# Kernel optimization log

Measured on AMD Instinct MI355X. Metric: run time of the kernel, lower is better.

The kernel has to match this reference:

```python
import jax, jax.numpy as jnp
import numpy as np

SEQ_LEN = 1024
D_MODEL = 512
K_FILT = 24
HEADS = 8
R = 512  # must equal d_model for the module's forward to type-check
NFFT = 2048  # nearest power of two >= 2*SEQ_LEN-1
LN_EPS = 1e-5


def _spectral_filters():
    # Hankel matrix Z[i,j] = 2 / ((i+j)^3 - (i+j)), i,j in 1..T
    e = np.arange(1, SEQ_LEN + 1, dtype=np.float64)
    ipj = e[:, None] + e[None, :]
    Z = 2.0 / (ipj ** 3 - ipj)
    sigma, phi = np.linalg.eigh(Z)
    sigma_k = np.clip(sigma[-K_FILT:], 1e-9, None)
    phi_k = phi[:, -K_FILT:] * sigma_k ** 0.25
    return phi_k.astype(np.float32)  # (T, K)


def setup_inputs() -> dict:
    key = jax.random.key(0)
    ks = jax.random.split(key, 12)
    s = 0.02
    B = 2

    def lin(k):
        kw, kb = jax.random.split(k)
        return (jax.random.normal(kw, (D_MODEL, D_MODEL), jnp.float32) * s,
                jax.random.normal(kb, (D_MODEL,), jnp.float32) * s)

    Wq, bq = lin(ks[0]); Wk, bk = lin(ks[1]); Wv, bv = lin(ks[2])
    Wg, bg = lin(ks[3]); Wo, bo = lin(ks[4])
    return {
        'x': jax.random.normal(ks[5], (B, SEQ_LEN, D_MODEL), jnp.float32),
        'stu_filters': jnp.asarray(_spectral_filters()),
        'M_inputs': jax.random.normal(ks[6], (D_MODEL, R), jnp.float32) * s,
        'M_filters': jax.random.normal(ks[7], (K_FILT, R), jnp.float32) * s,
        'Wq': Wq, 'bq': bq, 'Wk': Wk, 'bk': bk, 'Wv': Wv, 'bv': bv,
        'Wg': Wg, 'bg': bg, 'Wo': Wo, 'bo': bo,
        'ln_w': jnp.ones((R,), jnp.float32),
        'ln_b': jnp.zeros((R,), jnp.float32),
    }


def _stu_conv(u, v):
    # u: (B, T, r), v: (T, r). FFT-based causal conv with sign featurization.
    T = u.shape[1]
    sgn = jnp.where(jnp.arange(T) % 2 == 1, -1.0, 1.0)[None, :, None]  # (1,T,1)
    Vf = jnp.fft.rfft(v[None, :, :, None], n=NFFT, axis=1)  # (1,F,r,1)
    U = jnp.stack([u, u * sgn], axis=-1)  # (B,T,r,2)
    Uf = jnp.fft.rfft(U, n=NFFT, axis=1)  # (B,F,r,2)
    conv = jnp.fft.irfft(Vf * Uf, n=NFFT, axis=1)[:, :T]  # (B,T,r,2)
    return conv[..., 0], conv[..., 1] * sgn


def _layernorm(x, w, b):
    mu = jnp.mean(x, axis=-1, keepdims=True)
    var = jnp.mean((x - mu) ** 2, axis=-1, keepdims=True)
    return (x - mu) * jax.lax.rsqrt(var + LN_EPS) * w + b


def reference(x, stu_filters, M_inputs, M_filters, Wq, bq, Wk, bk, Wv, bv,
              Wg, bg, Wo, bo, ln_w, ln_b):
    B, T, d = x.shape
    hd = d // HEADS
    # STU features
    u_proj = x @ M_inputs                    # (B,T,r)
    phi_proj = stu_filters @ M_filters       # (T,r)
    sp, sm = _stu_conv(u_proj, phi_proj)
    x_tilde = _layernorm(sp + sm, ln_w, ln_b)  # (B,T,r==d)
    # gated linear attention with gelu features and causal cumsum state
    def proj(W, b):
        y = (x @ W.T + b).reshape(B, T, HEADS, hd).transpose(0, 2, 1, 3)
        return jax.nn.gelu(y, approximate=True)
    Q = proj(Wq, bq); K = proj(Wk, bk); V = proj(Wv, bv)
    Zt = jnp.einsum('bhtp,bhtn->bhtpn', V, K)   # (B,H,T,hd,hd)
    Hc = jnp.cumsum(Zt, axis=2)
    Y = jnp.einsum('bhtp,bhtpn->bhtn', Q, Hc)   # (B,H,T,hd)
    Y_attn = Y.transpose(0, 2, 1, 3).reshape(B, T, d)
    gate = jax.nn.sigmoid(x @ Wg.T + bg)
    comb = gate * Y_attn + (1.0 - gate) * x_tilde
    return comb @ Wo.T + bo
```

## Files before the change

### kernel.cpp

```cpp
#include <hip/hip_runtime.h>
#include <hip/hip_bf16.h>

#define T_SEQ 1024
#define D_MOD 512
#define NHEAD 8
#define HDIM  64
#define R_DIM 512
#define BATCH 2

typedef __attribute__((ext_vector_type(8))) __bf16 bf16x8;
typedef __attribute__((ext_vector_type(4))) float f32x4;

__device__ __forceinline__ float ldin(const void* p, size_t i, int bf) {
    if (bf) return __bfloat162float(((const __hip_bfloat16*)p)[i]);
    return ((const float*)p)[i];
}
__device__ __forceinline__ void stout(void* p, size_t i, int bf, float v) {
    if (bf) ((__hip_bfloat16*)p)[i] = __float2bfloat16(v);
    else    ((float*)p)[i] = v;
}

__device__ __forceinline__ float gelu_f(float x) {
    return 0.5f * x * (1.f + tanhf(0.7978845608028654f * (x + 0.044715f * x * x * x)));
}

__device__ __forceinline__ int detect_bf(const void* x) {
    __shared__ int cnt;
    if (threadIdx.x == 0) cnt = 0;
    __syncthreads();
    const unsigned short* h = (const unsigned short*)x;
    int c = 0;
    for (int i = threadIdx.x; i < 8192; i += 256)
        if ((h[i] & 0x7F80u) == 0x7F80u) c++;
    if (c) atomicAdd(&cnt, c);
    __syncthreads();
    return cnt == 0;
}

__global__ __launch_bounds__(256) void mega_gemm(
    const void* __restrict__ x, const void* __restrict__ Mi,
    const void* __restrict__ stf, const void* __restrict__ Mf,
    const void* __restrict__ Wq, const void* __restrict__ bq,
    const void* __restrict__ Wk, const void* __restrict__ bk,
    const void* __restrict__ Wv, const void* __restrict__ bv,
    const void* __restrict__ Wg, const void* __restrict__ bg,
    float* __restrict__ fu, float* __restrict__ fphi,
    __bf16* __restrict__ fQ, __bf16* __restrict__ fKT,
    __bf16* __restrict__ fV, __bf16* __restrict__ fG)
{
    const int tid = threadIdx.x;
    const int job = blockIdx.z;
    if (job == 6) {
        float4* zp = (float4*)(fphi + 524288);
        const int bid = blockIdx.y * 8 + blockIdx.x;
        const float4 z4 = make_float4(0.f, 0.f, 0.f, 0.f);
        #pragma unroll
        for (int q = 0; q < 8; ++q)
            zp[(size_t)bid * 2048 + q * 256 + tid] = z4;
        return;
    }
    const int bf = detect_bf(x);
    const void* A = x; const void* Bw; const void* bias = nullptr;
    int Kd = 512, act = 0; bool trb = true;
    switch (job) {
        case 0: Bw = Mi; trb = false; break;
        case 1: Bw = Wq; bias = bq; act = 1; break;
        case 2: Bw = Wk; bias = bk; act = 1; break;
        case 3: Bw = Wv; bias = bv; act = 1; break;
        case 4: Bw = Wg; bias = bg; act = 2; break;
        default: A = stf; Bw = Mf; trb = false; Kd = 32; break;
    }
    const int M = (job == 5) ? 1024 : 2048;
    const int m0 = blockIdx.y * 64;
    if (m0 >= M) return;
    const int n0 = blockIdx.x * 64;

    __shared__ __align__(16) __bf16 sm[2 * 64 * 40];
    __bf16 (*As)[40] = (__bf16 (*)[40])sm;
    __bf16 (*Bs)[40] = (__bf16 (*)[40])(sm + 64 * 40);
    const int wave = tid >> 6, lane = tid & 63;
    const int lm = lane & 15, kq = lane >> 4;

    f32x4 acc[4] = {};

    for (int k0 = 0; k0 < Kd; k0 += 32) {
        if (k0) __syncthreads();
        {
            const int mo = tid >> 2;
            const int ko = (tid & 3) * 8;
            if (job == 5) {
                bf16x8 t;
                #pragma unroll
                for (int q = 0; q < 8; ++q) {
                    const int k = ko + q;
                    t[q] = (k < 24) ? (__bf16)ldin(A, (size_t)(m0 + mo) * 24 + k, bf)
                                    : (__bf16)0.f;
                }
                *(bf16x8*)&As[mo][ko] = t;
            } else if (bf) {
                *(bf16x8*)&As[mo][ko] =
                    *(const bf16x8*)((const __bf16*)A + (size_t)(m0 + mo) * 512 + k0 + ko);
            } else {
                const float* Af = (const float*)A + (size_t)(m0 + mo) * 512 + k0 + ko;
                const float4 f0 = *(const float4*)Af;
                const float4 f1 = *(const float4*)(Af + 4);
                bf16x8 t;
                t[0]=(__bf16)f0.x; t[1]=(__bf16)f0.y; t[2]=(__bf16)f0.z; t[3]=(__bf16)f0.w;
                t[4]=(__bf16)f1.x; t[5]=(__bf16)f1.y; t[6]=(__bf16)f1.z; t[7]=(__bf16)f1.w;
                *(bf16x8*)&As[mo][ko] = t;
            }
        }
        if (trb) {
            const int no = tid >> 2;
            const int ko = (tid & 3) * 8;
            const size_t go = (size_t)(n0 + no) * 512 + k0 + ko;
            if (bf) {
                *(bf16x8*)&Bs[no][ko] = *(const bf16x8*)((const __bf16*)Bw + go);
            } else {
                const float* Bf = (const float*)Bw + go;
                const float4 f0 = *(const float4*)Bf;
                const float4 f1 = *(const float4*)(Bf + 4);
                bf16x8 t;
                t[0]=(__bf16)f0.x; t[1]=(__bf16)f0.y; t[2]=(__bf16)f0.z; t[3]=(__bf16)f0.w;
                t[4]=(__bf16)f1.x; t[5]=(__bf16)f1.y; t[6]=(__bf16)f1.z; t[7]=(__bf16)f1.w;
                *(bf16x8*)&Bs[no][ko] = t;
            }
        } else {
            const int n = tid & 63;
            const int kk = (tid >> 6) * 8;
            bf16x8 t;
            #pragma unroll
            for (int e = 0; e < 8; ++e) {
                const int k = k0 + kk + e;
                t[e] = (job == 5 && k >= 24) ? (__bf16)0.f
                     : (__bf16)ldin(Bw, (size_t)k * 512 + n0 + n, bf);
            }
            *(bf16x8*)&Bs[n][kk] = t;
        }
        __syncthreads();
        const bf16x8 a = *(const bf16x8*)&As[wave * 16 + lm][kq * 8];
        #pragma unroll
        for (int nt = 0; nt < 4; ++nt) {
            const bf16x8 b = *(const bf16x8*)&Bs[nt * 16 + lm][kq * 8];
            acc[nt] = __builtin_amdgcn_mfma_f32_16x16x32_bf16(a, b, acc[nt], 0, 0, 0);
        }
    }
    if (job == 2) {
        __syncthreads();
        __bf16 (*Kt)[72] = (__bf16 (*)[72])sm;
        #pragma unroll
        for (int nt = 0; nt < 4; ++nt) {
            const int n = nt * 16 + lm;
            #pragma unroll
            for (int r2 = 0; r2 < 4; ++r2) {
                float v = acc[nt][r2] + ldin(bias, (size_t)(n0 + n), bf);
                Kt[n][wave * 16 + kq * 4 + r2] = (__bf16)gelu_f(v);
            }
        }
        __syncthreads();
        const int h = n0 >> 6;
        const int b = m0 >> 10;
        const int tb = m0 & 1023;
        #pragma unroll
        for (int q = 0; q < 2; ++q) {
            const int c = q * 256 + tid;
            const int p = c >> 3, off = (c & 7) * 8;
            *(bf16x8*)&fKT[(((size_t)b * NHEAD + h) * 64 + p) * T_SEQ + tb + off] =
                *(const bf16x8*)&Kt[p][off];
        }
        return;
    }
    #pragma unroll
    for (int nt = 0; nt < 4; ++nt) {
        const int n = n0 + nt * 16 + lm;
        #pragma unroll
        for (int r2 = 0; r2 < 4; ++r2) {
            const int m = m0 + wave * 16 + kq * 4 + r2;
            float v = acc[nt][r2];
            if (bias) v += ldin(bias, (size_t)n, bf);
            if (act == 1) v = gelu_f(v);
            if (act == 2) v = 1.f / (1.f + expf(-v));
            switch (job) {
                case 0: fu[(size_t)m * 512 + n] = v; break;
                case 5: fphi[(size_t)m * 512 + n] = v; break;
                case 1: fQ[(size_t)m * 512 + n] = (__bf16)v; break;
                case 3: fV[(size_t)m * 512 + n] = (__bf16)v; break;
                default: fG[(size_t)m * 512 + n] = (__bf16)v; break;
            }
        }
    }
}

__global__ __launch_bounds__(256) void conv_attn_k(
    const float* __restrict__ u, const float* __restrict__ vphi,
    float* __restrict__ w,
    const __bf16* __restrict__ Q, const __bf16* __restrict__ KT,
    const __bf16* __restrict__ V, float* __restrict__ Y)
{
    __shared__ __align__(16) unsigned char smem[49152];
    const int tid = threadIdx.x;
    const int z = blockIdx.z;
    int rem = blockIdx.x, ti = 0;
    while (rem >= ((ti + 4) >> 2)) { rem -= (ti + 4) >> 2; ++ti; }
    const int jlo = rem * 4;
    const int jhi = (jlo + 3 < ti) ? jlo + 3 : ti;
    const int t0 = ti * 64;

    if (z < 2) {
        float (*vs)[64] = (float (*)[64])smem;
        float (*us)[64] = (float (*)[64])(smem + 16384);
        const int rl = tid & 63, tg = tid >> 6;
        const int b = z;
        const int r0 = blockIdx.y * 64;
        const float* ub = u + (size_t)b * T_SEQ * R_DIM;
        float acc[16] = {};
        for (int j = jlo; j <= jhi; ++j) {
            if (j != jlo) __syncthreads();
            const int L0 = j * 64;
            const int W0 = t0 - L0 - 63;
            #pragma unroll
            for (int jj = 0; jj < 8; ++jj) {
                const int n = jj * 256 + tid;
                const int row = n >> 4, c4 = (n & 15) * 4;
                int s = W0 + row;
                s = s < 0 ? 0 : (s > T_SEQ - 1 ? T_SEQ - 1 : s);
                *(float4*)&us[row][c4] = *(const float4*)&ub[(size_t)s * R_DIM + r0 + c4];
            }
            #pragma unroll
            for (int jj = 0; jj < 4; ++jj) {
                const int n = jj * 256 + tid;
                const int row = n >> 4, c4 = (n & 15) * 4;
                *(float4*)&vs[row][c4] = *(const float4*)&vphi[(size_t)(L0 + row) * R_DIM + r0 + c4];
            }
            __syncthreads();
            if (j < ti) {
                #pragma unroll
                for (int g = 0; g < 4; ++g) {
                    const int wsmin = tg * 16 + 49 - 16 * g;
                    float ur[30];
                    #pragma unroll
                    for (int q = 0; q < 30; ++q) ur[q] = us[wsmin + q][rl];
                    float vr[8];
                    #pragma unroll
                    for (int e = 0; e < 8; ++e) vr[e] = vs[16 * g + 2 * e][rl];
                    #pragma unroll
                    for (int e = 0; e < 8; ++e)
                        #pragma unroll
                        for (int i = 0; i < 16; ++i)
                            acc[i] += vr[e] * ur[i - 2 * e + 14];
                }
            } else {
                for (int l = 0; l < 64; l += 2) {
                    const float vv = vs[l][rl];
                    #pragma unroll
                    for (int i = 0; i < 16; ++i) {
                        const int srel = tg * 16 + i - l;
                        if (srel >= 0) acc[i] += vv * us[srel + 63][rl];
                    }
                }
            }
        }
        #pragma unroll
        for (int i = 0; i < 16; ++i)
            atomicAdd(&w[((size_t)b * T_SEQ + t0 + tg * 16 + i) * R_DIM + r0 + rl],
                      2.f * acc[i]);
    } else {
        __bf16 (*Qs)[72] = (__bf16 (*)[72])smem;
        __bf16 (*Vs)[72] = (__bf16 (*)[72])(smem + 9216);
        __bf16 (*Kt)[72] = (__bf16 (*)[72])(smem + 18432);
        __bf16 (*Sa)[72] = (__bf16 (*)[72])(smem + 27648);
        const int wave = tid >> 6, lane = tid & 63;
        const int lm = lane & 15, kq = lane >> 4;
        const int b = z - 2;
        const int h = blockIdx.y;
        const size_t cbase = ((size_t)b * T_SEQ) * D_MOD + h * HDIM;
        const __bf16* KTh = KT + (((size_t)b * NHEAD + h) * 64) * T_SEQ;
        #pragma unroll
        for (int it = 0; it < 2; ++it) {
            const int n = it * 256 + tid;
            const int row = n >> 3, p0 = (n & 7) * 8;
            *(bf16x8*)&Qs[row][p0] = *(const bf16x8*)&Q[cbase + (size_t)(t0 + row) * D_MOD + p0];
        }
        f32x4 accY[4] = {};
        for (int j = jlo; j <= jhi; ++j) {
            const int s0 = j * 64;
            __syncthreads();
            #pragma unroll
            for (int it = 0; it < 2; ++it) {
                const int n = it * 256 + tid;
                const int row = n >> 3, c0 = (n & 7) * 8;
                *(bf16x8*)&Vs[row][c0] = *(const bf16x8*)&V[cbase + (size_t)(s0 + row) * D_MOD + c0];
                *(bf16x8*)&Kt[row][c0] = *(const bf16x8*)&KTh[(size_t)row * T_SEQ + s0 + c0];
            }
            __syncthreads();
            f32x4 sacc[4] = {};
            #pragma unroll
            for (int ks = 0; ks < 2; ++ks) {
                const bf16x8 a = *(const bf16x8*)&Qs[wave * 16 + lm][ks * 32 + kq * 8];
                #pragma unroll
                for (int nt = 0; nt < 4; ++nt) {
                    const bf16x8 bb = *(const bf16x8*)&Vs[nt * 16 + lm][ks * 32 + kq * 8];
                    sacc[nt] = __builtin_amdgcn_mfma_f32_16x16x32_bf16(a, bb, sacc[nt], 0, 0, 0);
                }
            }
            const bool diag = (j == ti);
            #pragma unroll
            for (int nt = 0; nt < 4; ++nt) {
                const int sl = nt * 16 + lm;
                #pragma unroll
                for (int r2 = 0; r2 < 4; ++r2) {
                    const int tl = wave * 16 + kq * 4 + r2;
                    float v = sacc[nt][r2];
                    if (diag && sl > tl) v = 0.f;
                    Sa[tl][sl] = (__bf16)v;
                }
            }
            #pragma unroll
            for (int ks = 0; ks < 2; ++ks) {
                const bf16x8 a = *(const bf16x8*)&Sa[wave * 16 + lm][ks * 32 + kq * 8];
                #pragma unroll
                for (int nt = 0; nt < 4; ++nt) {
                    const bf16x8 bb = *(const bf16x8*)&Kt[nt * 16 + lm][ks * 32 + kq * 8];
                    accY[nt] = __builtin_amdgcn_mfma_f32_16x16x32_bf16(a, bb, accY[nt], 0, 0, 0);
                }
            }
        }
        #pragma unroll
        for (int nt = 0; nt < 4; ++nt) {
            const int nh = nt * 16 + lm;
            #pragma unroll
            for (int r2 = 0; r2 < 4; ++r2) {
                const int tl = wave * 16 + kq * 4 + r2;
                atomicAdd(&Y[cbase + (size_t)(t0 + tl) * D_MOD + nh], accY[nt][r2]);
            }
        }
    }
}

__global__ __launch_bounds__(256) void ln_k(float* __restrict__ w,
                                            const void* __restrict__ g,
                                            const void* __restrict__ b,
                                            const void* __restrict__ xref)
{
    const int bf = detect_bf(xref);
    const size_t row = (size_t)blockIdx.y * T_SEQ + blockIdx.x;
    float* p = w + row * R_DIM;
    const int tid = threadIdx.x;
    const float x0 = p[tid], x1 = p[tid + 256];
    __shared__ float red[4];
    float s = x0 + x1;
    #pragma unroll
    for (int off = 32; off > 0; off >>= 1) s += __shfl_down(s, off, 64);
    if ((tid & 63) == 0) red[tid >> 6] = s;
    __syncthreads();
    const float mu = (red[0] + red[1] + red[2] + red[3]) * (1.f / 512.f);
    __syncthreads();
    const float d0 = x0 - mu, d1 = x1 - mu;
    float vsum = d0 * d0 + d1 * d1;
    #pragma unroll
    for (int off = 32; off > 0; off >>= 1) vsum += __shfl_down(vsum, off, 64);
    if ((tid & 63) == 0) red[tid >> 6] = vsum;
    __syncthreads();
    const float var = (red[0] + red[1] + red[2] + red[3]) * (1.f / 512.f);
    const float rs = rsqrtf(var + 1e-5f);
    p[tid]       = d0 * rs * ldin(g, tid, bf)       + ldin(b, tid, bf);
    p[tid + 256] = d1 * rs * ldin(g, tid + 256, bf) + ldin(b, tid + 256, bf);
}

__global__ __launch_bounds__(256) void final_gemm(const __bf16* __restrict__ G,
                                                  const float* __restrict__ Yf,
                                                  const float* __restrict__ Xt,
                                                  const void* __restrict__ Wo,
                                                  const void* __restrict__ bo,
                                                  void* __restrict__ out,
                                                  const void* __restrict__ xref)
{
    const int bf = detect_bf(xref);
    __shared__ __align__(16) __bf16 As[64][40];
    __shared__ __align__(16) __bf16 Bs[64][40];
    const int tid = threadIdx.x;
    const int wave = tid >> 6, lane = tid & 63;
    const int lm = lane & 15, kq = lane >> 4;
    const int m0 = blockIdx.y * 64, n0 = blockIdx.x * 64;

    f32x4 acc[4] = {};

    for (int k0 = 0; k0 < 512; k0 += 32) {
        __syncthreads();
        {
            const int mo = tid >> 2;
            const int ko = (tid & 3) * 8;
            const size_t off = (size_t)(m0 + mo) * 512 + k0 + ko;
            const bf16x8 g8 = *(const bf16x8*)(G + off);
            const float4 y0 = *(const float4*)(Yf + off);
            const float4 y1 = *(const float4*)(Yf + off + 4);
            const float4 x0 = *(const float4*)(Xt + off);
            const float4 x1 = *(const float4*)(Xt + off + 4);
            const float yv[8] = {y0.x,y0.y,y0.z,y0.w,y1.x,y1.y,y1.z,y1.w};
            const float xv[8] = {x0.x,x0.y,x0.z,x0.w,x1.x,x1.y,x1.z,x1.w};
            bf16x8 t;
            #pragma unroll
            for (int q = 0; q < 8; ++q) {
                const float gg = (float)g8[q];
                t[q] = (__bf16)(gg * yv[q] + (1.f - gg) * xv[q]);
            }
            *(bf16x8*)&As[mo][ko] = t;
        }
        {
            const int no = tid >> 2;
            const int ko = (tid & 3) * 8;
            const size_t off = (size_t)(n0 + no) * 512 + k0 + ko;
            if (bf) {
                *(bf16x8*)&Bs[no][ko] = *(const bf16x8*)((const __bf16*)Wo + off);
            } else {
                const float* Bf = (const float*)Wo + off;
                const float4 f0 = *(const float4*)Bf;
                const float4 f1 = *(const float4*)(Bf + 4);
                bf16x8 t;
                t[0]=(__bf16)f0.x; t[1]=(__bf16)f0.y; t[2]=(__bf16)f0.z; t[3]=(__bf16)f0.w;
                t[4]=(__bf16)f1.x; t[5]=(__bf16)f1.y; t[6]=(__bf16)f1.z; t[7]=(__bf16)f1.w;
                *(bf16x8*)&Bs[no][ko] = t;
            }
        }
        __syncthreads();
        const bf16x8 a = *(const bf16x8*)&As[wave * 16 + lm][kq * 8];
        #pragma unroll
        for (int nt = 0; nt < 4; ++nt) {
            const bf16x8 b = *(const bf16x8*)&Bs[nt * 16 + lm][kq * 8];
            acc[nt] = __builtin_amdgcn_mfma_f32_16x16x32_bf16(a, b, acc[nt], 0, 0, 0);
        }
    }
    #pragma unroll
    for (int nt = 0; nt < 4; ++nt) {
        const int n = n0 + nt * 16 + lm;
        #pragma unroll
        for (int r2 = 0; r2 < 4; ++r2) {
            const int m = m0 + wave * 16 + kq * 4 + r2;
            float v = acc[nt][r2] + ldin(bo, (size_t)n, bf);
            stout(out, (size_t)m * 512 + n, bf, v);
        }
    }
}

extern "C" void kernel_launch(void* const* d_in, const int* in_sizes, int n_in,
                              void* d_out, int out_size, void* d_ws, size_t ws_size,
                              hipStream_t stream)
{
    const void* x   = d_in[0];
    const void* stf = d_in[1];
    const void* Mi  = d_in[2];
    const void* Mf  = d_in[3];
    const void* Wq  = d_in[4];  const void* bq = d_in[5];
    const void* Wk  = d_in[6];  const void* bk = d_in[7];
    const void* Wv  = d_in[8];  const void* bv = d_in[9];
    const void* Wg  = d_in[10]; const void* bg = d_in[11];
    const void* Wo  = d_in[12]; const void* bo = d_in[13];
    const void* lnw = d_in[14]; const void* lnb = d_in[15];

    float* base = (float*)d_ws;
    float*  f_u   = base;
    float*  f_phi = base + 1048576;
    float*  f_w   = base + 1572864;
    float*  f_Y   = base + 2621440;
    __bf16* f_Q   = (__bf16*)(base + 3670016);
    __bf16* f_KT  = f_Q + 1048576;
    __bf16* f_V   = f_KT + 1048576;
    __bf16* f_G   = f_V + 1048576;

    dim3 blk(256);

    mega_gemm<<<dim3(8, 32, 7), blk, 0, stream>>>(
        x, Mi, stf, Mf, Wq, bq, Wk, bk, Wv, bv, Wg, bg,
        f_u, f_phi, f_Q, f_KT, f_V, f_G);

    conv_attn_k<<<dim3(40, 8, 4), blk, 0, stream>>>(f_u, f_phi, f_w, f_Q, f_KT, f_V, f_Y);

    ln_k<<<dim3(T_SEQ, BATCH), blk, 0, stream>>>(f_w, lnw, lnb, x);

    final_gemm<<<dim3(8, 32), blk, 0, stream>>>(f_G, f_Y, f_w, Wo, bo, d_out, x);
}
```

Before: 204.2 us.

## Double-buffer LDS tiles and prefetch next K-slice in GEMM kernels

Both the multi-job projection GEMM and the final gated GEMM now use two shared-memory tile buffers. Global loads for the next K-slice are issued into registers before the MFMAs on the current slice, then written to the other buffer afterwards, with one barrier per iteration instead of two. This hides global-load latency behind compute, at the cost of twice the LDS and more live registers.

```diff
diff --git a/kernel.cpp b/kernel.cpp
--- a/kernel.cpp
+++ b/kernel.cpp
@@ -22,6 +22,13 @@
 
 __device__ __forceinline__ float gelu_f(float x) {
     return 0.5f * x * (1.f + tanhf(0.7978845608028654f * (x + 0.044715f * x * x * x)));
+}
+
+__device__ __forceinline__ bf16x8 cvt8(float4 a, float4 b) {
+    bf16x8 t;
+    t[0]=(__bf16)a.x; t[1]=(__bf16)a.y; t[2]=(__bf16)a.z; t[3]=(__bf16)a.w;
+    t[4]=(__bf16)b.x; t[5]=(__bf16)b.y; t[6]=(__bf16)b.z; t[7]=(__bf16)b.w;
+    return t;
 }
 
 __device__ __forceinline__ int detect_bf(const void* x) {
@@ -75,79 +82,86 @@
     if (m0 >= M) return;
     const int n0 = blockIdx.x * 64;
 
-    __shared__ __align__(16) __bf16 sm[2 * 64 * 40];
-    __bf16 (*As)[40] = (__bf16 (*)[40])sm;
-    __bf16 (*Bs)[40] = (__bf16 (*)[40])(sm + 64 * 40);
+    __shared__ __align__(16) __bf16 sm[2][2 * 64 * 40];
     const int wave = tid >> 6, lane = tid & 63;
     const int lm = lane & 15, kq = lane >> 4;
-
-    f32x4 acc[4] = {};
-
-    for (int k0 = 0; k0 < Kd; k0 += 32) {
-        if (k0) __syncthreads();
-        {
-            const int mo = tid >> 2;
-            const int ko = (tid & 3) * 8;
-            if (job == 5) {
-                bf16x8 t;
-                #pragma unroll
-                for (int q = 0; q < 8; ++q) {
-                    const int k = ko + q;
-                    t[q] = (k < 24) ? (__bf16)ldin(A, (size_t)(m0 + mo) * 24 + k, bf)
-                                    : (__bf16)0.f;
-                }
-                *(bf16x8*)&As[mo][ko] = t;
-            } else if (bf) {
-                *(bf16x8*)&As[mo][ko] =
-                    *(const bf16x8*)((const __bf16*)A + (size_t)(m0 + mo) * 512 + k0 + ko);
-            } else {
-                const float* Af = (const float*)A + (size_t)(m0 + mo) * 512 + k0 + ko;
-                const float4 f0 = *(const float4*)Af;
-                const float4 f1 = *(const float4*)(Af + 4);
-                bf16x8 t;
-                t[0]=(__bf16)f0.x; t[1]=(__bf16)f0.y; t[2]=(__bf16)f0.z; t[3]=(__bf16)f0.w;
-                t[4]=(__bf16)f1.x; t[5]=(__bf16)f1.y; t[6]=(__bf16)f1.z; t[7]=(__bf16)f1.w;
-                *(bf16x8*)&As[mo][ko] = t;
-            }
+    const int mo = tid >> 2, ko = (tid & 3) * 8;
+    const int gn = tid & 63, gk = (tid >> 6) * 8;
+
+    bf16x8 ba, bb;
+    float4 fa0, fa1, fb0, fb1;
+
+    auto issue = [&](int k0) {
+        if (job == 5) {
+            bf16x8 t;
+            #pragma unroll
+            for (int q = 0; q < 8; ++q) {
+                const int k = ko + q;
+                t[q] = (k < 24) ? (__bf16)ldin(A, (size_t)(m0 + mo) * 24 + k, bf)
+                                : (__bf16)0.f;
+            }
+            ba = t;
+        } else if (bf) {
+            ba = *(const bf16x8*)((const __bf16*)A + (size_t)(m0 + mo) * 512 + k0 + ko);
+        } else {
+            const float* Af = (const float*)A + (size_t)(m0 + mo) * 512 + k0 + ko;
+            fa0 = *(const float4*)Af; fa1 = *(const float4*)(Af + 4);
         }
         if (trb) {
-            const int no = tid >> 2;
-            const int ko = (tid & 3) * 8;
-            const size_t go = (size_t)(n0 + no) * 512 + k0 + ko;
+            const size_t go = (size_t)(n0 + mo) * 512 + k0 + ko;
             if (bf) {
-                *(bf16x8*)&Bs[no][ko] = *(const bf16x8*)((const __bf16*)Bw + go);
+                bb = *(const bf16x8*)((const __bf16*)Bw + go);
             } else {
                 const float* Bf = (const float*)Bw + go;
-                const float4 f0 = *(const float4*)Bf;
-                const float4 f1 = *(const float4*)(Bf + 4);
-                bf16x8 t;
-                t[0]=(__bf16)f0.x; t[1]=(__bf16)f0.y; t[2]=(__bf16)f0.z; t[3]=(__bf16)f0.w;
-                t[4]=(__bf16)f1.x; t[5]=(__bf16)f1.y; t[6]=(__bf16)f1.z; t[7]=(__bf16)f1.w;
-                *(bf16x8*)&Bs[no][ko] = t;
+                fb0 = *(const float4*)Bf; fb1 = *(const float4*)(Bf + 4);
             }
         } else {
-            const int n = tid & 63;
-            const int kk = (tid >> 6) * 8;
             bf16x8 t;
             #pragma unroll
             for (int e = 0; e < 8; ++e) {
-                const int k = k0 + kk + e;
+                const int k = k0 + gk + e;
                 t[e] = (job == 5 && k >= 24) ? (__bf16)0.f
-                     : (__bf16)ldin(Bw, (size_t)k * 512 + n0 + n, bf);
-            }
-            *(bf16x8*)&Bs[n][kk] = t;
-        }
-        __syncthreads();
+                     : (__bf16)ldin(Bw, (size_t)k * 512 + n0 + gn, bf);
+            }
+            bb = t;
+        }
+    };
+    auto commit = [&](int bi) {
+        __bf16 (*As)[40] = (__bf16 (*)[40])sm[bi];
+        __bf16 (*Bs)[40] = (__bf16 (*)[40])(sm[bi] + 64 * 40);
+        bf16x8 va = ba, vb = bb;
+        if (job != 5 && !bf) va = cvt8(fa0, fa1);
+        if (trb && !bf)      vb = cvt8(fb0, fb1);
+        *(bf16x8*)&As[mo][ko] = va;
+        if (trb) *(bf16x8*)&Bs[mo][ko] = vb;
+        else     *(bf16x8*)&Bs[gn][gk] = vb;
+    };
+
+    f32x4 acc[4] = {};
+    issue(0);
+    commit(0);
+    __syncthreads();
+    int cur = 0;
+    for (int k0 = 0; k0 < Kd; k0 += 32) {
+        const bool haveNext = (k0 + 32 < Kd);
+        if (haveNext) issue(k0 + 32);
+        __bf16 (*As)[40] = (__bf16 (*)[40])sm[cur];
+        __bf16 (*Bs)[40] = (__bf16 (*)[40])(sm[cur] + 64 * 40);
         const bf16x8 a = *(const bf16x8*)&As[wave * 16 + lm][kq * 8];
         #pragma unroll
         for (int nt = 0; nt < 4; ++nt) {
             const bf16x8 b = *(const bf16x8*)&Bs[nt * 16 + lm][kq * 8];
             acc[nt] = __builtin_amdgcn_mfma_f32_16x16x32_bf16(a, b, acc[nt], 0, 0, 0);
         }
+        if (haveNext) {
+            commit(cur ^ 1);
+            __syncthreads();
+            cur ^= 1;
+        }
     }
     if (job == 2) {
         __syncthreads();
-        __bf16 (*Kt)[72] = (__bf16 (*)[72])sm;
+        __bf16 (*Kt)[72] = (__bf16 (*)[72])sm[0];
         #pragma unroll
         for (int nt = 0; nt < 4; ++nt) {
             const int n = nt * 16 + lm;
@@ -376,58 +390,61 @@
                                                   const void* __restrict__ xref)
 {
     const int bf = detect_bf(xref);
-    __shared__ __align__(16) __bf16 As[64][40];
-    __shared__ __align__(16) __bf16 Bs[64][40];
+    __shared__ __align__(16) __bf16 sm[2][2 * 64 * 40];
     const int tid = threadIdx.x;
     const int wave = tid >> 6, lane = tid & 63;
     const int lm = lane & 15, kq = lane >> 4;
+    const int mo = tid >> 2, ko = (tid & 3) * 8;
     const int m0 = blockIdx.y * 64, n0 = blockIdx.x * 64;
 
+    bf16x8 pg, pw;
+    float4 py0, py1, px0, px1, pw0, pw1;
+
+    auto issue = [&](int k0) {
+        const size_t off = (size_t)(m0 + mo) * 512 + k0 + ko;
+        pg  = *(const bf16x8*)(G + off);
+        py0 = *(const float4*)(Yf + off); py1 = *(const float4*)(Yf + off + 4);
+        px0 = *(const float4*)(Xt + off); px1 = *(const float4*)(Xt + off + 4);
+        const size_t ob = (size_t)(n0 + mo) * 512 + k0 + ko;
+        if (bf) pw = *(const bf16x8*)((const __bf16*)Wo + ob);
+        else { const float* Bf = (const float*)Wo + ob;
+               pw0 = *(const float4*)Bf; pw1 = *(const float4*)(Bf + 4); }
+    };
+    auto commit = [&](int bi) {
+        __bf16 (*As)[40] = (__bf16 (*)[40])sm[bi];
+        __bf16 (*Bs)[40] = (__bf16 (*)[40])(sm[bi] + 64 * 40);
+        const float yv[8] = {py0.x,py0.y,py0.z,py0.w,py1.x,py1.y,py1.z,py1.w};
+        const float xv[8] = {px0.x,px0.y,px0.z,px0.w,px1.x,px1.y,px1.z,px1.w};
+        bf16x8 t;
+        #pragma unroll
+        for (int q = 0; q < 8; ++q) {
+            const float gg = (float)pg[q];
+            t[q] = (__bf16)(gg * yv[q] + (1.f - gg) * xv[q]);
+        }
+        *(bf16x8*)&As[mo][ko] = t;
+        *(bf16x8*)&Bs[mo][ko] = bf ? pw : cvt8(pw0, pw1);
+    };
+
     f32x4 acc[4] = {};
-
+    issue(0);
+    commit(0);
+    __syncthreads();
+    int cur = 0;
     for (int k0 = 0; k0 < 512; k0 += 32) {
-        __syncthreads();
-        {
-            const int mo = tid >> 2;
-            const int ko = (tid & 3) * 8;
-            const size_t off = (size_t)(m0 + mo) * 512 + k0 + ko;
-            const bf16x8 g8 = *(const bf16x8*)(G + off);
-            const float4 y0 = *(const float4*)(Yf + off);
-            const float4 y1 = *(const float4*)(Yf + off + 4);
-            const float4 x0 = *(const float4*)(Xt + off);
-            const float4 x1 = *(const float4*)(Xt + off + 4);
-            const float yv[8] = {y0.x,y0.y,y0.z,y0.w,y1.x,y1.y,y1.z,y1.w};
-            const float xv[8] = {x0.x,x0.y,x0.z,x0.w,x1.x,x1.y,x1.z,x1.w};
-            bf16x8 t;
-            #pragma unroll
-            for (int q = 0; q < 8; ++q) {
-                const float gg = (float)g8[q];
-                t[q] = (__bf16)(gg * yv[q] + (1.f - gg) * xv[q]);
-            }
-            *(bf16x8*)&As[mo][ko] = t;
-        }
-        {
-            const int no = tid >> 2;
-            const int ko = (tid & 3) * 8;
-            const size_t off = (size_t)(n0 + no) * 512 + k0 + ko;
-            if (bf) {
-                *(bf16x8*)&Bs[no][ko] = *(const bf16x8*)((const __bf16*)Wo + off);
-            } else {
-                const float* Bf = (const float*)Wo + off;
-                const float4 f0 = *(const float4*)Bf;
-                const float4 f1 = *(const float4*)(Bf + 4);
-                bf16x8 t;
-                t[0]=(__bf16)f0.x; t[1]=(__bf16)f0.y; t[2]=(__bf16)f0.z; t[3]=(__bf16)f0.w;
-                t[4]=(__bf16)f1.x; t[5]=(__bf16)f1.y; t[6]=(__bf16)f1.z; t[7]=(__bf16)f1.w;
-                *(bf16x8*)&Bs[no][ko] = t;
-            }
-        }
-        __syncthreads();
+        const bool haveNext = (k0 + 32 < 512);
+        if (haveNext) issue(k0 + 32);
+        __bf16 (*As)[40] = (__bf16 (*)[40])sm[cur];
+        __bf16 (*Bs)[40] = (__bf16 (*)[40])(sm[cur] + 64 * 40);
         const bf16x8 a = *(const bf16x8*)&As[wave * 16 + lm][kq * 8];
         #pragma unroll
         for (int nt = 0; nt < 4; ++nt) {
             const bf16x8 b = *(const bf16x8*)&Bs[nt * 16 + lm][kq * 8];
             acc[nt] = __builtin_amdgcn_mfma_f32_16x16x32_bf16(a, b, acc[nt], 0, 0, 0);
+        }
+        if (haveNext) {
+            commit(cur ^ 1);
+            __syncthreads();
+            cur ^= 1;
         }
     }
     #pragma unroll
```

Result: no change. 202.4 us (-0.9%).
